# Kernel optimization log

Hardware: AMD Instinct MI355X
Metric: run time of the kernel (lower is better)

Reference implementation:

```python
import jax, jax.numpy as jnp
import numpy as np

V, C, H, W = 6, 256, 128, 128


def setup_inputs() -> dict:
    key = jax.random.key(0)
    ks = jax.random.split(key, 6)
    return {
        "q": jax.random.normal(ks[0], (V, C, H, W), dtype=jnp.float32),
        "k": jax.random.normal(ks[1], (V, C, H, W), dtype=jnp.float32),
        "v": jax.random.normal(ks[2], (V, C, H, W), dtype=jnp.float32),
        "Wq": jax.random.normal(ks[3], (C, C), dtype=jnp.float32) * (1.0 / np.sqrt(C)),
        "Wk": jax.random.normal(ks[4], (C, C), dtype=jnp.float32) * (1.0 / np.sqrt(C)),
        "Wv": jax.random.normal(ks[5], (C, C), dtype=jnp.float32) * (1.0 / np.sqrt(C)),
    }


def reference(q, k, v, Wq, Wk, Wv):
    # 1x1 conv (no bias) == channel GEMM: [V,C,H,W] x [O,C] -> [V,O,H,W]
    qp = jnp.einsum("vchw,oc->vohw", q, Wq)
    kp = jnp.einsum("vchw,oc->vohw", k, Wk)
    vp = jnp.einsum("vchw,oc->vohw", v, Wv)
    # elementwise q*k, sum over channels (dim=1, keepdim) -> [V,1,H,W]
    att = jnp.sum(qp * kp, axis=1, keepdims=True)
    # softmax over views (dim=0)
    att = jax.nn.softmax(att, axis=0)
    # weight values and sum over views (dim=0, keepdim) -> [1,C,H,W]
    out = jnp.sum(att * vp, axis=0, keepdims=True)
    return out
```

## Files before the change

### kernel.cpp

```cpp
#include <hip/hip_runtime.h>
#include <math.h>

#define HW 16384
#define C_DIM 256
#define V_DIM 6
#define PT 64
#define BK 32
#define KROW 40
#define KT (PT * KROW)

typedef short bf16x8 __attribute__((ext_vector_type(8)));
typedef float f32x4 __attribute__((ext_vector_type(4)));

__device__ __forceinline__ void split2(float x, unsigned short& h,
                                       unsigned short& l) {
    unsigned u = __float_as_uint(x);
    h = (unsigned short)(u >> 16);
    float xl = x - __uint_as_float(u & 0xFFFF0000u);
    l = (unsigned short)(__float_as_uint(xl) >> 16);
}

__global__ void compute_M_kernel(const float* __restrict__ Wq,
                                 const float* __restrict__ Wk,
                                 unsigned short* __restrict__ Mh,
                                 unsigned short* __restrict__ Ml) {
    const int i = blockIdx.x;
    const int j = threadIdx.x;
    float a0 = 0.f, a1 = 0.f, a2 = 0.f, a3 = 0.f;
    #pragma unroll 4
    for (int o = 0; o < C_DIM; o += 4) {
        a0 = fmaf(Wq[(o + 0) * C_DIM + i], Wk[(o + 0) * C_DIM + j], a0);
        a1 = fmaf(Wq[(o + 1) * C_DIM + i], Wk[(o + 1) * C_DIM + j], a1);
        a2 = fmaf(Wq[(o + 2) * C_DIM + i], Wk[(o + 2) * C_DIM + j], a2);
        a3 = fmaf(Wq[(o + 3) * C_DIM + i], Wk[(o + 3) * C_DIM + j], a3);
    }
    float acc = (a0 + a1) + (a2 + a3);
    unsigned short h, l;
    split2(acc, h, l);
    Mh[i * C_DIM + j] = h;
    Ml[i * C_DIM + j] = l;
}

__global__ __launch_bounds__(512, 4) void score_kernel(
        const float* __restrict__ q, const float* __restrict__ k,
        const unsigned short* __restrict__ Mh,
        const unsigned short* __restrict__ Ml,
        float* __restrict__ score) {
    const int tid  = threadIdx.x;
    const int lane = tid & 63;
    const int w    = tid >> 6;
    const int pt   = blockIdx.x & 255;
    const int v    = blockIdx.x >> 8;
    const int gp0  = pt * PT;
    const int l15  = lane & 15;
    const int l4   = lane >> 4;

    __shared__ __align__(16) unsigned short Kh_s[8 * KT];
    __shared__ __align__(16) unsigned short Kl_s[8 * KT];

    const float* kv = k + (size_t)v * C_DIM * HW + gp0;
    const float* qv = q + (size_t)v * C_DIM * HW + gp0;
    const int ibase = w * 32;

    {
        float kx[8][4];
        #pragma unroll
        for (int t = 0; t < 8; ++t) {
            const float* kp = kv + (size_t)(t * BK + w * 4) * HW + lane;
            #pragma unroll
            for (int e = 0; e < 4; ++e) kx[t][e] = kp[(size_t)e * HW];
        }
        #pragma unroll
        for (int t = 0; t < 8; ++t) {
            unsigned short h[4], l[4];
            #pragma unroll
            for (int e = 0; e < 4; ++e) split2(kx[t][e], h[e], l[e]);
            uint2 H, L;
            H.x = (unsigned)h[0] | ((unsigned)h[1] << 16);
            H.y = (unsigned)h[2] | ((unsigned)h[3] << 16);
            L.x = (unsigned)l[0] | ((unsigned)l[1] << 16);
            L.y = (unsigned)l[2] | ((unsigned)l[3] << 16);
            *(uint2*)&Kh_s[t * KT + lane * KROW + w * 4] = H;
            *(uint2*)&Kl_s[t * KT + lane * KROW + w * 4] = L;
        }
    }
    __syncthreads();

    f32x4 acc[2][4];
    #pragma unroll
    for (int a = 0; a < 2; ++a)
        #pragma unroll
        for (int b = 0; b < 4; ++b)
            acc[a][b] = (f32x4){0.f, 0.f, 0.f, 0.f};

    bf16x8 Ah[2][2], Al[2][2];
    #pragma unroll
    for (int it = 0; it < 2; ++it) {
        int row = ibase + it * 16 + l15;
        Ah[0][it] = *(const bf16x8*)(Mh + (size_t)row * C_DIM + l4 * 8);
        Al[0][it] = *(const bf16x8*)(Ml + (size_t)row * C_DIM + l4 * 8);
    }

    #pragma unroll
    for (int ks = 0; ks < 8; ++ks) {
        const int cur = ks & 1;

        if (ks < 7) {
            #pragma unroll
            for (int it = 0; it < 2; ++it) {
                int row = ibase + it * 16 + l15;
                Ah[cur ^ 1][it] = *(const bf16x8*)(Mh + (size_t)row * C_DIM +
                                                   (ks + 1) * BK + l4 * 8);
                Al[cur ^ 1][it] = *(const bf16x8*)(Ml + (size_t)row * C_DIM +
                                                   (ks + 1) * BK + l4 * 8);
            }
        }

        bf16x8 Bh[4];
        #pragma unroll
        for (int jt = 0; jt < 4; ++jt) {
            int bp = jt * 16 + l15;
            Bh[jt] = *(const bf16x8*)&Kh_s[ks * KT + bp * KROW + l4 * 8];
        }
        #pragma unroll
        for (int it = 0; it < 2; ++it)
            #pragma unroll
            for (int jt = 0; jt < 4; ++jt)
                acc[it][jt] = __builtin_amdgcn_mfma_f32_16x16x32_bf16(
                                  Ah[cur][it], Bh[jt], acc[it][jt], 0, 0, 0);
        #pragma unroll
        for (int it = 0; it < 2; ++it)
            #pragma unroll
            for (int jt = 0; jt < 4; ++jt)
                acc[it][jt] = __builtin_amdgcn_mfma_f32_16x16x32_bf16(
                                  Al[cur][it], Bh[jt], acc[it][jt], 0, 0, 0);
        bf16x8 Bl[4];
        #pragma unroll
        for (int jt = 0; jt < 4; ++jt) {
            int bp = jt * 16 + l15;
            Bl[jt] = *(const bf16x8*)&Kl_s[ks * KT + bp * KROW + l4 * 8];
        }
        #pragma unroll
        for (int it = 0; it < 2; ++it)
            #pragma unroll
            for (int jt = 0; jt < 4; ++jt)
                acc[it][jt] = __builtin_amdgcn_mfma_f32_16x16x32_bf16(
                                  Ah[cur][it], Bl[jt], acc[it][jt], 0, 0, 0);
    }

    float sp[4];
    #pragma unroll
    for (int jt = 0; jt < 4; ++jt) sp[jt] = 0.f;
    #pragma unroll
    for (int jt = 0; jt < 4; ++jt) {
        #pragma unroll
        for (int it = 0; it < 2; ++it) {
            int irow = ibase + it * 16 + l4 * 4;
            const float* qp = qv + (size_t)irow * HW + jt * 16 + l15;
            #pragma unroll
            for (int r = 0; r < 4; ++r)
                sp[jt] = fmaf(qp[(size_t)r * HW], acc[it][jt][r], sp[jt]);
        }
        sp[jt] += __shfl_xor(sp[jt], 16, 64);
        sp[jt] += __shfl_xor(sp[jt], 32, 64);
    }

    __syncthreads();
    float* s_red = (float*)Kh_s;
    if (lane < 16) {
        #pragma unroll
        for (int jt = 0; jt < 4; ++jt)
            s_red[w * PT + jt * 16 + lane] = sp[jt];
    }
    __syncthreads();
    if (tid < PT) {
        float s = 0.f;
        #pragma unroll
        for (int ww = 0; ww < 8; ++ww) s += s_red[ww * PT + tid];
        score[v * HW + gp0 + tid] = s;
    }
}

__global__ void wsplit_kernel(const float* __restrict__ Wv,
                              unsigned short* __restrict__ Wvh,
                              unsigned short* __restrict__ Wvl) {
    const int i = blockIdx.x;
    const int j = threadIdx.x;
    unsigned short h, l;
    split2(Wv[i * C_DIM + j], h, l);
    Wvh[i * C_DIM + j] = h;
    Wvl[i * C_DIM + j] = l;
}

__global__ __launch_bounds__(512, 2) void out_gemm_kernel(
        const float* __restrict__ vin,
        const unsigned short* __restrict__ Wvh,
        const unsigned short* __restrict__ Wvl,
        const float* __restrict__ score,
        float* __restrict__ out) {
    const int tid  = threadIdx.x;
    const int lane = tid & 63;
    const int w    = tid >> 6;
    const int gp0  = blockIdx.x * PT;
    const int l15  = lane & 15;
    const int l4   = lane >> 4;
    const int jg   = w;

    __shared__ __align__(16) unsigned short Xh_s[2][KT];
    __shared__ __align__(16) unsigned short Xl_s[2][KT];

    float wr[V_DIM];
    {
        float s[V_DIM];
        float mx = -1e30f;
        #pragma unroll
        for (int vv = 0; vv < V_DIM; ++vv) {
            s[vv] = score[vv * HW + gp0 + lane];
            mx = fmaxf(mx, s[vv]);
        }
        float sum = 0.f;
        #pragma unroll
        for (int vv = 0; vv < V_DIM; ++vv) {
            s[vv] = __expf(s[vv] - mx);
            sum += s[vv];
        }
        float inv = 1.0f / sum;
        #pragma unroll
        for (int vv = 0; vv < V_DIM; ++vv) wr[vv] = s[vv] * inv;
    }

    const float* vbase = vin + gp0 + lane;
    const int obase = w * 32;

    f32x4 acc[2][4];
    #pragma unroll
    for (int a = 0; a < 2; ++a)
        #pragma unroll
        for (int b = 0; b < 4; ++b)
            acc[a][b] = (f32x4){0.f, 0.f, 0.f, 0.f};

    float vx[2][4][V_DIM];
    bf16x8 Ah[2][2], Al[2][2];

    {
        float x0[4][V_DIM];
        #pragma unroll
        for (int vv = 0; vv < V_DIM; ++vv)
            #pragma unroll
            for (int e = 0; e < 4; ++e)
                x0[e][vv] = vbase[(size_t)(vv * C_DIM + jg * 4 + e) * HW];
        unsigned short h[4], l[4];
        #pragma unroll
        for (int e = 0; e < 4; ++e) {
            float s = 0.f;
            #pragma unroll
            for (int vv = 0; vv < V_DIM; ++vv) s = fmaf(wr[vv], x0[e][vv], s);
            split2(s, h[e], l[e]);
        }
        uint2 H, L;
        H.x = (unsigned)h[0] | ((unsigned)h[1] << 16);
        H.y = (unsigned)h[2] | ((unsigned)h[3] << 16);
        L.x = (unsigned)l[0] | ((unsigned)l[1] << 16);
        L.y = (unsigned)l[2] | ((unsigned)l[3] << 16);
        *(uint2*)&Xh_s[0][lane * KROW + jg * 4] = H;
        *(uint2*)&Xl_s[0][lane * KROW + jg * 4] = L;

        #pragma unroll
        for (int vv = 0; vv < V_DIM; ++vv)
            #pragma unroll
            for (int e = 0; e < 4; ++e)
                vx[1][e][vv] = vbase[(size_t)(vv * C_DIM + BK + jg * 4 + e) * HW];

        #pragma unroll
        for (int it = 0; it < 2; ++it) {
            int row = obase + it * 16 + l15;
            Ah[0][it] = *(const bf16x8*)(Wvh + (size_t)row * C_DIM + l4 * 8);
            Al[0][it] = *(const bf16x8*)(Wvl + (size_t)row * C_DIM + l4 * 8);
        }
    }
    __syncthreads();

    #pragma unroll
    for (int ks = 0; ks < 8; ++ks) {
        const int cur = ks & 1;

        if (ks < 7) {
            #pragma unroll
            for (int it = 0; it < 2; ++it) {
                int row = obase + it * 16 + l15;
                Ah[cur ^ 1][it] = *(const bf16x8*)(Wvh + (size_t)row * C_DIM +
                                                   (ks + 1) * BK + l4 * 8);
                Al[cur ^ 1][it] = *(const bf16x8*)(Wvl + (size_t)row * C_DIM +
                                                   (ks + 1) * BK + l4 * 8);
            }
        }
        if (ks < 6) {
            #pragma unroll
            for (int vv = 0; vv < V_DIM; ++vv)
                #pragma unroll
                for (int e = 0; e < 4; ++e)
                    vx[cur][e][vv] = vbase[(size_t)(vv * C_DIM + (ks + 2) * BK +
                                                    jg * 4 + e) * HW];
        }

        bf16x8 Bh[4], Bl[4];
        #pragma unroll
        for (int jt = 0; jt < 4; ++jt) {
            int bp = jt * 16 + l15;
            Bh[jt] = *(const bf16x8*)&Xh_s[cur][bp * KROW + l4 * 8];
            Bl[jt] = *(const bf16x8*)&Xl_s[cur][bp * KROW + l4 * 8];
        }
        #pragma unroll
        for (int it = 0; it < 2; ++it)
            #pragma unroll
            for (int jt = 0; jt < 4; ++jt)
                acc[it][jt] = __builtin_amdgcn_mfma_f32_16x16x32_bf16(
                                  Ah[cur][it], Bh[jt], acc[it][jt], 0, 0, 0);
        #pragma unroll
        for (int it = 0; it < 2; ++it)
            #pragma unroll
            for (int jt = 0; jt < 4; ++jt)
                acc[it][jt] = __builtin_amdgcn_mfma_f32_16x16x32_bf16(
                                  Ah[cur][it], Bl[jt], acc[it][jt], 0, 0, 0);
        #pragma unroll
        for (int it = 0; it < 2; ++it)
            #pragma unroll
            for (int jt = 0; jt < 4; ++jt)
                acc[it][jt] = __builtin_amdgcn_mfma_f32_16x16x32_bf16(
                                  Al[cur][it], Bh[jt], acc[it][jt], 0, 0, 0);

        if (ks < 7) {
            unsigned short h[4], l[4];
            #pragma unroll
            for (int e = 0; e < 4; ++e) {
                float s = 0.f;
                #pragma unroll
                for (int vv = 0; vv < V_DIM; ++vv)
                    s = fmaf(wr[vv], vx[cur ^ 1][e][vv], s);
                split2(s, h[e], l[e]);
            }
            uint2 H, L;
            H.x = (unsigned)h[0] | ((unsigned)h[1] << 16);
            H.y = (unsigned)h[2] | ((unsigned)h[3] << 16);
            L.x = (unsigned)l[0] | ((unsigned)l[1] << 16);
            L.y = (unsigned)l[2] | ((unsigned)l[3] << 16);
            *(uint2*)&Xh_s[cur ^ 1][lane * KROW + jg * 4] = H;
            *(uint2*)&Xl_s[cur ^ 1][lane * KROW + jg * 4] = L;
        }
        __syncthreads();
    }

    #pragma unroll
    for (int it = 0; it < 2; ++it)
        #pragma unroll
        for (int jt = 0; jt < 4; ++jt)
            #pragma unroll
            for (int r = 0; r < 4; ++r) {
                int o = obase + it * 16 + l4 * 4 + r;
                out[(size_t)o * HW + gp0 + jt * 16 + l15] = acc[it][jt][r];
            }
}

extern "C" void kernel_launch(void* const* d_in, const int* in_sizes, int n_in,
                              void* d_out, int out_size, void* d_ws, size_t ws_size,
                              hipStream_t stream) {
    const float* q  = (const float*)d_in[0];
    const float* k  = (const float*)d_in[1];
    const float* v  = (const float*)d_in[2];
    const float* Wq = (const float*)d_in[3];
    const float* Wk = (const float*)d_in[4];
    const float* Wv = (const float*)d_in[5];
    float* out = (float*)d_out;

    unsigned short* Mh = (unsigned short*)d_ws;
    unsigned short* Ml = Mh + C_DIM * C_DIM;
    float* score = (float*)(Ml + C_DIM * C_DIM);

    compute_M_kernel<<<C_DIM, C_DIM, 0, stream>>>(Wq, Wk, Mh, Ml);
    score_kernel<<<V_DIM * 256, 512, 0, stream>>>(q, k, Mh, Ml, score);
    wsplit_kernel<<<C_DIM, C_DIM, 0, stream>>>(Wv, Mh, Ml);
    out_gemm_kernel<<<HW / PT, 512, 0, stream>>>(v, Mh, Ml, score, out);
}
```

Measured before the change: 121.9 us.

## Restructure score kernel to stage M tiles in LDS with 4-wave blocks

The score kernel now runs 256-thread blocks, each wave computing a 64x64 output tile. Each K-step stages the M hi/lo slice in shared memory instead of having every wave stream M fragments from global memory, and the K hi/lo split is done per K-step rather than all up front. The aim is to cut global/L2 traffic for M, since each loaded M fragment now feeds more MFMAs per wave. The cost is a per-step load-then-barrier pattern with no double buffering, a larger accumulator register footprint, and more LDS per block (about 46 KB), which may lower occupancy.

```diff
diff --git a/kernel.cpp b/kernel.cpp
--- a/kernel.cpp
+++ b/kernel.cpp
@@ -6,8 +6,7 @@
 #define V_DIM 6
 #define PT 64
 #define BK 32
-#define KROW 40
-#define KT (PT * KROW)
+#define MROW 40
 
 typedef short bf16x8 __attribute__((ext_vector_type(8)));
 typedef float f32x4 __attribute__((ext_vector_type(4)));
@@ -41,7 +40,7 @@
     Ml[i * C_DIM + j] = l;
 }
 
-__global__ __launch_bounds__(512, 4) void score_kernel(
+__global__ __launch_bounds__(256) void score_kernel(
         const float* __restrict__ q, const float* __restrict__ k,
         const unsigned short* __restrict__ Mh,
         const unsigned short* __restrict__ Ml,
@@ -54,98 +53,88 @@
     const int gp0  = pt * PT;
     const int l15  = lane & 15;
     const int l4   = lane >> 4;
-
-    __shared__ __align__(16) unsigned short Kh_s[8 * KT];
-    __shared__ __align__(16) unsigned short Kl_s[8 * KT];
+    const int p_s  = tid & 63;
+    const int jg   = tid >> 6;
+
+    __shared__ __align__(16) unsigned short Mh_s[C_DIM * MROW];
+    __shared__ __align__(16) unsigned short Ml_s[C_DIM * MROW];
+    __shared__ __align__(16) unsigned short Kh_s[PT * MROW];
+    __shared__ __align__(16) unsigned short Kl_s[PT * MROW];
+    __shared__ float s_red[4][PT];
 
     const float* kv = k + (size_t)v * C_DIM * HW + gp0;
     const float* qv = q + (size_t)v * C_DIM * HW + gp0;
-    const int ibase = w * 32;
-
-    {
-        float kx[8][4];
-        #pragma unroll
-        for (int t = 0; t < 8; ++t) {
-            const float* kp = kv + (size_t)(t * BK + w * 4) * HW + lane;
-            #pragma unroll
-            for (int e = 0; e < 4; ++e) kx[t][e] = kp[(size_t)e * HW];
-        }
-        #pragma unroll
-        for (int t = 0; t < 8; ++t) {
-            unsigned short h[4], l[4];
-            #pragma unroll
-            for (int e = 0; e < 4; ++e) split2(kx[t][e], h[e], l[e]);
-            uint2 H, L;
+
+    f32x4 acc[4][4];
+    #pragma unroll
+    for (int a = 0; a < 4; ++a)
+        #pragma unroll
+        for (int b = 0; b < 4; ++b)
+            acc[a][b] = (f32x4){0.f, 0.f, 0.f, 0.f};
+
+    const int ibase = w * 64;
+
+    for (int ks = 0; ks < C_DIM / BK; ++ks) {
+        const int j0 = ks * BK;
+
+        #pragma unroll
+        for (int e = 0; e < 4; ++e) {
+            int cidx = tid + 256 * e;
+            int i  = cidx >> 2;
+            int jb = cidx & 3;
+            uint4 mh = *(const uint4*)(Mh + i * C_DIM + j0 + jb * 8);
+            uint4 ml = *(const uint4*)(Ml + i * C_DIM + j0 + jb * 8);
+            *(uint4*)&Mh_s[i * MROW + jb * 8] = mh;
+            *(uint4*)&Ml_s[i * MROW + jb * 8] = ml;
+        }
+
+        {
+            const float* kp = kv + (size_t)(j0 + jg * 8) * HW + p_s;
+            float x[8];
+            #pragma unroll
+            for (int e = 0; e < 8; ++e) x[e] = kp[(size_t)e * HW];
+            unsigned short h[8], l[8];
+            #pragma unroll
+            for (int e = 0; e < 8; ++e) split2(x[e], h[e], l[e]);
+            uint4 H, L;
             H.x = (unsigned)h[0] | ((unsigned)h[1] << 16);
             H.y = (unsigned)h[2] | ((unsigned)h[3] << 16);
+            H.z = (unsigned)h[4] | ((unsigned)h[5] << 16);
+            H.w = (unsigned)h[6] | ((unsigned)h[7] << 16);
             L.x = (unsigned)l[0] | ((unsigned)l[1] << 16);
             L.y = (unsigned)l[2] | ((unsigned)l[3] << 16);
-            *(uint2*)&Kh_s[t * KT + lane * KROW + w * 4] = H;
-            *(uint2*)&Kl_s[t * KT + lane * KROW + w * 4] = L;
-        }
-    }
-    __syncthreads();
-
-    f32x4 acc[2][4];
-    #pragma unroll
-    for (int a = 0; a < 2; ++a)
-        #pragma unroll
-        for (int b = 0; b < 4; ++b)
-            acc[a][b] = (f32x4){0.f, 0.f, 0.f, 0.f};
-
-    bf16x8 Ah[2][2], Al[2][2];
-    #pragma unroll
-    for (int it = 0; it < 2; ++it) {
-        int row = ibase + it * 16 + l15;
-        Ah[0][it] = *(const bf16x8*)(Mh + (size_t)row * C_DIM + l4 * 8);
-        Al[0][it] = *(const bf16x8*)(Ml + (size_t)row * C_DIM + l4 * 8);
-    }
-
-    #pragma unroll
-    for (int ks = 0; ks < 8; ++ks) {
-        const int cur = ks & 1;
-
-        if (ks < 7) {
-            #pragma unroll
-            for (int it = 0; it < 2; ++it) {
-                int row = ibase + it * 16 + l15;
-                Ah[cur ^ 1][it] = *(const bf16x8*)(Mh + (size_t)row * C_DIM +
-                                                   (ks + 1) * BK + l4 * 8);
-                Al[cur ^ 1][it] = *(const bf16x8*)(Ml + (size_t)row * C_DIM +
-                                                   (ks + 1) * BK + l4 * 8);
-            }
-        }
-
-        bf16x8 Bh[4];
+            L.z = (unsigned)l[4] | ((unsigned)l[5] << 16);
+            L.w = (unsigned)l[6] | ((unsigned)l[7] << 16);
+            *(uint4*)&Kh_s[p_s * MROW + jg * 8] = H;
+            *(uint4*)&Kl_s[p_s * MROW + jg * 8] = L;
+        }
+        __syncthreads();
+
+        bf16x8 Ah[4], Al[4], Bh[4], Bl[4];
+        #pragma unroll
+        for (int it = 0; it < 4; ++it) {
+            int ai = ibase + it * 16 + l15;
+            Ah[it] = *(const bf16x8*)&Mh_s[ai * MROW + l4 * 8];
+            Al[it] = *(const bf16x8*)&Ml_s[ai * MROW + l4 * 8];
+        }
         #pragma unroll
         for (int jt = 0; jt < 4; ++jt) {
             int bp = jt * 16 + l15;
-            Bh[jt] = *(const bf16x8*)&Kh_s[ks * KT + bp * KROW + l4 * 8];
-        }
-        #pragma unroll
-        for (int it = 0; it < 2; ++it)
-            #pragma unroll
-            for (int jt = 0; jt < 4; ++jt)
-                acc[it][jt] = __builtin_amdgcn_mfma_f32_16x16x32_bf16(
-                                  Ah[cur][it], Bh[jt], acc[it][jt], 0, 0, 0);
-        #pragma unroll
-        for (int it = 0; it < 2; ++it)
-            #pragma unroll
-            for (int jt = 0; jt < 4; ++jt)
-                acc[it][jt] = __builtin_amdgcn_mfma_f32_16x16x32_bf16(
-                                  Al[cur][it], Bh[jt], acc[it][jt], 0, 0, 0);
-        bf16x8 Bl[4];
-        #pragma unroll
-        for (int jt = 0; jt < 4; ++jt) {
-            int bp = jt * 16 + l15;
-            Bl[jt] = *(const bf16x8*)&Kl_s[ks * KT + bp * KROW + l4 * 8];
-        }
-        #pragma unroll
-        for (int it = 0; it < 2; ++it)
-            #pragma unroll
-            for (int jt = 0; jt < 4; ++jt)
-                acc[it][jt] = __builtin_amdgcn_mfma_f32_16x16x32_bf16(
-                                  Ah[cur][it], Bl[jt], acc[it][jt], 0, 0, 0);
+            Bh[jt] = *(const bf16x8*)&Kh_s[bp * MROW + l4 * 8];
+            Bl[jt] = *(const bf16x8*)&Kl_s[bp * MROW + l4 * 8];
+        }
+        #pragma unroll
+        for (int it = 0; it < 4; ++it)
+            #pragma unroll
+            for (int jt = 0; jt < 4; ++jt) {
+                acc[it][jt] = __builtin_amdgcn_mfma_f32_16x16x32_bf16(
+                                  Ah[it], Bh[jt], acc[it][jt], 0, 0, 0);
+                acc[it][jt] = __builtin_amdgcn_mfma_f32_16x16x32_bf16(
+                                  Ah[it], Bl[jt], acc[it][jt], 0, 0, 0);
+                acc[it][jt] = __builtin_amdgcn_mfma_f32_16x16x32_bf16(
+                                  Al[it], Bh[jt], acc[it][jt], 0, 0, 0);
+            }
+        __syncthreads();
     }
 
     float sp[4];
@@ -154,7 +143,7 @@
     #pragma unroll
     for (int jt = 0; jt < 4; ++jt) {
         #pragma unroll
-        for (int it = 0; it < 2; ++it) {
+        for (int it = 0; it < 4; ++it) {
             int irow = ibase + it * 16 + l4 * 4;
             const float* qp = qv + (size_t)irow * HW + jt * 16 + l15;
             #pragma unroll
@@ -164,20 +153,15 @@
         sp[jt] += __shfl_xor(sp[jt], 16, 64);
         sp[jt] += __shfl_xor(sp[jt], 32, 64);
     }
-
-    __syncthreads();
-    float* s_red = (float*)Kh_s;
     if (lane < 16) {
         #pragma unroll
         for (int jt = 0; jt < 4; ++jt)
-            s_red[w * PT + jt * 16 + lane] = sp[jt];
+            s_red[w][jt * 16 + lane] = sp[jt];
     }
     __syncthreads();
     if (tid < PT) {
-        float s = 0.f;
-        #pragma unroll
-        for (int ww = 0; ww < 8; ++ww) s += s_red[ww * PT + tid];
-        score[v * HW + gp0 + tid] = s;
+        score[v * HW + gp0 + tid] =
+            s_red[0][tid] + s_red[1][tid] + s_red[2][tid] + s_red[3][tid];
     }
 }
 
@@ -192,6 +176,8 @@
     Wvl[i * C_DIM + j] = l;
 }
 
+#define KROW 40
+#define KT (PT * KROW)
 __global__ __launch_bounds__(512, 2) void out_gemm_kernel(
         const float* __restrict__ vin,
         const unsigned short* __restrict__ Wvh,
@@ -377,7 +363,7 @@
     float* score = (float*)(Ml + C_DIM * C_DIM);
 
     compute_M_kernel<<<C_DIM, C_DIM, 0, stream>>>(Wq, Wk, Mh, Ml);
-    score_kernel<<<V_DIM * 256, 512, 0, stream>>>(q, k, Mh, Ml, score);
+    score_kernel<<<V_DIM * 256, 256, 0, stream>>>(q, k, Mh, Ml, score);
     wsplit_kernel<<<C_DIM, C_DIM, 0, stream>>>(Wv, Mh, Ml);
     out_gemm_kernel<<<HW / PT, 512, 0, stream>>>(v, Mh, Ml, score, out);
 }
```

Measured after the change: 124.8 us. 2.4% more time.

## Loop score kernel over views per block and prefetch next view's k into registers

Applied to the files above, without the earlier changes.

The score kernel now launches one block per 64-pixel tile and loops over all six views inside the block, rather than launching one block per (view, tile). While the MFMA work for the current view runs, the next view's k slice is loaded into registers, and q values are loaded ahead of the reduction. This aims to hide global load latency and reuse the M fragments' cache locality. In exchange, grid size drops from 1536 to 256 blocks and the occupancy hint drops to 2, which may leave CUs underused and raise register pressure.

```diff
diff --git a/kernel.cpp b/kernel.cpp
--- a/kernel.cpp
+++ b/kernel.cpp
@@ -41,7 +41,7 @@
     Ml[i * C_DIM + j] = l;
 }
 
-__global__ __launch_bounds__(512, 4) void score_kernel(
+__global__ __launch_bounds__(512, 2) void score_kernel(
         const float* __restrict__ q, const float* __restrict__ k,
         const unsigned short* __restrict__ Mh,
         const unsigned short* __restrict__ Ml,
@@ -49,32 +49,36 @@
     const int tid  = threadIdx.x;
     const int lane = tid & 63;
     const int w    = tid >> 6;
-    const int pt   = blockIdx.x & 255;
-    const int v    = blockIdx.x >> 8;
-    const int gp0  = pt * PT;
+    const int gp0  = blockIdx.x * PT;
     const int l15  = lane & 15;
     const int l4   = lane >> 4;
 
     __shared__ __align__(16) unsigned short Kh_s[8 * KT];
     __shared__ __align__(16) unsigned short Kl_s[8 * KT];
 
-    const float* kv = k + (size_t)v * C_DIM * HW + gp0;
-    const float* qv = q + (size_t)v * C_DIM * HW + gp0;
     const int ibase = w * 32;
 
+    float kreg[8][4];
     {
-        float kx[8][4];
+        const float* kv = k + gp0;
         #pragma unroll
         for (int t = 0; t < 8; ++t) {
             const float* kp = kv + (size_t)(t * BK + w * 4) * HW + lane;
             #pragma unroll
-            for (int e = 0; e < 4; ++e) kx[t][e] = kp[(size_t)e * HW];
-        }
+            for (int e = 0; e < 4; ++e) kreg[t][e] = kp[(size_t)e * HW];
+        }
+    }
+
+    for (int v = 0; v < V_DIM; ++v) {
+        const float* qv = q + (size_t)v * C_DIM * HW + gp0;
+
+        if (v > 0) __syncthreads();
+
         #pragma unroll
         for (int t = 0; t < 8; ++t) {
             unsigned short h[4], l[4];
             #pragma unroll
-            for (int e = 0; e < 4; ++e) split2(kx[t][e], h[e], l[e]);
+            for (int e = 0; e < 4; ++e) split2(kreg[t][e], h[e], l[e]);
             uint2 H, L;
             H.x = (unsigned)h[0] | ((unsigned)h[1] << 16);
             H.y = (unsigned)h[2] | ((unsigned)h[3] << 16);
@@ -83,101 +87,118 @@
             *(uint2*)&Kh_s[t * KT + lane * KROW + w * 4] = H;
             *(uint2*)&Kl_s[t * KT + lane * KROW + w * 4] = L;
         }
-    }
-    __syncthreads();
-
-    f32x4 acc[2][4];
-    #pragma unroll
-    for (int a = 0; a < 2; ++a)
-        #pragma unroll
-        for (int b = 0; b < 4; ++b)
-            acc[a][b] = (f32x4){0.f, 0.f, 0.f, 0.f};
-
-    bf16x8 Ah[2][2], Al[2][2];
-    #pragma unroll
-    for (int it = 0; it < 2; ++it) {
-        int row = ibase + it * 16 + l15;
-        Ah[0][it] = *(const bf16x8*)(Mh + (size_t)row * C_DIM + l4 * 8);
-        Al[0][it] = *(const bf16x8*)(Ml + (size_t)row * C_DIM + l4 * 8);
-    }
-
-    #pragma unroll
-    for (int ks = 0; ks < 8; ++ks) {
-        const int cur = ks & 1;
-
-        if (ks < 7) {
+        __syncthreads();
+
+        float qx[32];
+        #pragma unroll
+        for (int jt = 0; jt < 4; ++jt)
             #pragma unroll
             for (int it = 0; it < 2; ++it) {
-                int row = ibase + it * 16 + l15;
-                Ah[cur ^ 1][it] = *(const bf16x8*)(Mh + (size_t)row * C_DIM +
-                                                   (ks + 1) * BK + l4 * 8);
-                Al[cur ^ 1][it] = *(const bf16x8*)(Ml + (size_t)row * C_DIM +
-                                                   (ks + 1) * BK + l4 * 8);
-            }
-        }
-
-        bf16x8 Bh[4];
+                int irow = ibase + it * 16 + l4 * 4;
+                const float* qp = qv + (size_t)irow * HW + jt * 16 + l15;
+                #pragma unroll
+                for (int r = 0; r < 4; ++r)
+                    qx[jt * 8 + it * 4 + r] = qp[(size_t)r * HW];
+            }
+        if (v < V_DIM - 1) {
+            const float* kv = k + (size_t)(v + 1) * C_DIM * HW + gp0;
+            #pragma unroll
+            for (int t = 0; t < 8; ++t) {
+                const float* kp = kv + (size_t)(t * BK + w * 4) * HW + lane;
+                #pragma unroll
+                for (int e = 0; e < 4; ++e) kreg[t][e] = kp[(size_t)e * HW];
+            }
+        }
+
+        f32x4 acc[2][4];
+        #pragma unroll
+        for (int a = 0; a < 2; ++a)
+            #pragma unroll
+            for (int b = 0; b < 4; ++b)
+                acc[a][b] = (f32x4){0.f, 0.f, 0.f, 0.f};
+
+        bf16x8 Ah[2][2], Al[2][2];
+        #pragma unroll
+        for (int it = 0; it < 2; ++it) {
+            int row = ibase + it * 16 + l15;
+            Ah[0][it] = *(const bf16x8*)(Mh + (size_t)row * C_DIM + l4 * 8);
+            Al[0][it] = *(const bf16x8*)(Ml + (size_t)row * C_DIM + l4 * 8);
+        }
+
+        #pragma unroll
+        for (int ks = 0; ks < 8; ++ks) {
+            const int cur = ks & 1;
+            if (ks < 7) {
+                #pragma unroll
+                for (int it = 0; it < 2; ++it) {
+                    int row = ibase + it * 16 + l15;
+                    Ah[cur ^ 1][it] = *(const bf16x8*)(Mh + (size_t)row * C_DIM +
+                                                       (ks + 1) * BK + l4 * 8);
+                    Al[cur ^ 1][it] = *(const bf16x8*)(Ml + (size_t)row * C_DIM +
+                                                       (ks + 1) * BK + l4 * 8);
+                }
+            }
+            bf16x8 Bh[4];
+            #pragma unroll
+            for (int jt = 0; jt < 4; ++jt) {
+                int bp = jt * 16 + l15;
+                Bh[jt] = *(const bf16x8*)&Kh_s[ks * KT + bp * KROW + l4 * 8];
+            }
+            #pragma unroll
+            for (int it = 0; it < 2; ++it)
+                #pragma unroll
+                for (int jt = 0; jt < 4; ++jt)
+                    acc[it][jt] = __builtin_amdgcn_mfma_f32_16x16x32_bf16(
+                                      Ah[cur][it], Bh[jt], acc[it][jt], 0, 0, 0);
+            #pragma unroll
+            for (int it = 0; it < 2; ++it)
+                #pragma unroll
+                for (int jt = 0; jt < 4; ++jt)
+                    acc[it][jt] = __builtin_amdgcn_mfma_f32_16x16x32_bf16(
+                                      Al[cur][it], Bh[jt], acc[it][jt], 0, 0, 0);
+            bf16x8 Bl[4];
+            #pragma unroll
+            for (int jt = 0; jt < 4; ++jt) {
+                int bp = jt * 16 + l15;
+                Bl[jt] = *(const bf16x8*)&Kl_s[ks * KT + bp * KROW + l4 * 8];
+            }
+            #pragma unroll
+            for (int it = 0; it < 2; ++it)
+                #pragma unroll
+                for (int jt = 0; jt < 4; ++jt)
+                    acc[it][jt] = __builtin_amdgcn_mfma_f32_16x16x32_bf16(
+                                      Ah[cur][it], Bl[jt], acc[it][jt], 0, 0, 0);
+        }
+
+        float sp[4];
+        #pragma unroll
+        for (int jt = 0; jt < 4; ++jt) sp[jt] = 0.f;
         #pragma unroll
         for (int jt = 0; jt < 4; ++jt) {
-            int bp = jt * 16 + l15;
-            Bh[jt] = *(const bf16x8*)&Kh_s[ks * KT + bp * KROW + l4 * 8];
-        }
-        #pragma unroll
-        for (int it = 0; it < 2; ++it)
+            #pragma unroll
+            for (int it = 0; it < 2; ++it)
+                #pragma unroll
+                for (int r = 0; r < 4; ++r)
+                    sp[jt] = fmaf(qx[jt * 8 + it * 4 + r],
+                                  acc[it][jt][r], sp[jt]);
+            sp[jt] += __shfl_xor(sp[jt], 16, 64);
+            sp[jt] += __shfl_xor(sp[jt], 32, 64);
+        }
+
+        __syncthreads();
+        float* s_red = (float*)Kh_s;
+        if (lane < 16) {
             #pragma unroll
             for (int jt = 0; jt < 4; ++jt)
-                acc[it][jt] = __builtin_amdgcn_mfma_f32_16x16x32_bf16(
-                                  Ah[cur][it], Bh[jt], acc[it][jt], 0, 0, 0);
-        #pragma unroll
-        for (int it = 0; it < 2; ++it)
-            #pragma unroll
-            for (int jt = 0; jt < 4; ++jt)
-                acc[it][jt] = __builtin_amdgcn_mfma_f32_16x16x32_bf16(
-                                  Al[cur][it], Bh[jt], acc[it][jt], 0, 0, 0);
-        bf16x8 Bl[4];
-        #pragma unroll
-        for (int jt = 0; jt < 4; ++jt) {
-            int bp = jt * 16 + l15;
-            Bl[jt] = *(const bf16x8*)&Kl_s[ks * KT + bp * KROW + l4 * 8];
-        }
-        #pragma unroll
-        for (int it = 0; it < 2; ++it)
-            #pragma unroll
-            for (int jt = 0; jt < 4; ++jt)
-                acc[it][jt] = __builtin_amdgcn_mfma_f32_16x16x32_bf16(
-                                  Ah[cur][it], Bl[jt], acc[it][jt], 0, 0, 0);
-    }
-
-    float sp[4];
-    #pragma unroll
-    for (int jt = 0; jt < 4; ++jt) sp[jt] = 0.f;
-    #pragma unroll
-    for (int jt = 0; jt < 4; ++jt) {
-        #pragma unroll
-        for (int it = 0; it < 2; ++it) {
-            int irow = ibase + it * 16 + l4 * 4;
-            const float* qp = qv + (size_t)irow * HW + jt * 16 + l15;
-            #pragma unroll
-            for (int r = 0; r < 4; ++r)
-                sp[jt] = fmaf(qp[(size_t)r * HW], acc[it][jt][r], sp[jt]);
-        }
-        sp[jt] += __shfl_xor(sp[jt], 16, 64);
-        sp[jt] += __shfl_xor(sp[jt], 32, 64);
-    }
-
-    __syncthreads();
-    float* s_red = (float*)Kh_s;
-    if (lane < 16) {
-        #pragma unroll
-        for (int jt = 0; jt < 4; ++jt)
-            s_red[w * PT + jt * 16 + lane] = sp[jt];
-    }
-    __syncthreads();
-    if (tid < PT) {
-        float s = 0.f;
-        #pragma unroll
-        for (int ww = 0; ww < 8; ++ww) s += s_red[ww * PT + tid];
-        score[v * HW + gp0 + tid] = s;
+                s_red[w * PT + jt * 16 + lane] = sp[jt];
+        }
+        __syncthreads();
+        if (tid < PT) {
+            float s = 0.f;
+            #pragma unroll
+            for (int ww = 0; ww < 8; ++ww) s += s_red[ww * PT + tid];
+            score[v * HW + gp0 + tid] = s;
+        }
     }
 }
 
@@ -377,7 +398,7 @@
     float* score = (float*)(Ml + C_DIM * C_DIM);
 
     compute_M_kernel<<<C_DIM, C_DIM, 0, stream>>>(Wq, Wk, Mh, Ml);
-    score_kernel<<<V_DIM * 256, 512, 0, stream>>>(q, k, Mh, Ml, score);
+    score_kernel<<<HW / PT, 512, 0, stream>>>(q, k, Mh, Ml, score);
     wsplit_kernel<<<C_DIM, C_DIM, 0, stream>>>(Wv, Mh, Ml);
     out_gemm_kernel<<<HW / PT, 512, 0, stream>>>(v, Mh, Ml, score, out);
 }
```

After: 109.6 us. 10.1% less time.
